# Kernel optimization log

Measured on AMD Instinct MI355X. Metric: run time of the kernel, lower is better.

## Reference

```python
import jax, jax.numpy as jnp
import numpy as np

B, S, D, H = 8, 2048, 1024, 8
CHUNK = D // H
SCALE = float(D) ** (-0.5)  # key_dim ** -0.5, key_dim == num_units here
LN_EPS = 1e-5


def setup_inputs() -> dict:
    key = jax.random.key(0)
    ks = jax.random.split(key, 9)
    s = 0.02
    return {
        "query": jax.random.normal(ks[0], (B, S, D), jnp.float32),
        "keys": jax.random.normal(ks[1], (B, S, D), jnp.float32),
        "Wq": jax.random.normal(ks[2], (D, D), jnp.float32) * s,  # torch Linear weight [out,in]
        "Wk": jax.random.normal(ks[3], (D, D), jnp.float32) * s,
        "Wv": jax.random.normal(ks[4], (D, D), jnp.float32) * s,
        "Wp": jax.random.normal(ks[5], (D, D), jnp.float32) * s,
        "bp": jnp.zeros((D,), jnp.float32),
        "ln_gamma": jnp.ones((D,), jnp.float32),
        "ln_beta": jnp.zeros((D,), jnp.float32),
    }


def reference(query, keys, Wq, Wk, Wv, Wp, bp, ln_gamma, ln_beta):
    # Linear layers (no bias on q/k/v): y = x @ W.T
    Q = jnp.einsum("bsd,ed->bse", query, Wq)
    K = jnp.einsum("bsd,ed->bse", keys, Wk)
    V = jnp.einsum("bsd,ed->bse", keys, Wv)
    # Faithful to original: raw view to [B*h, S, chunk] (no transpose head split)
    Qh = Q.reshape(B * H, S, CHUNK)
    Kh = K.reshape(B * H, S, CHUNK)
    Vh = V.reshape(B * H, S, CHUNK)
    # scores [B*h, S, S], scale, softmax (is_masked=False, dropout_p=0)
    att = jnp.einsum("gqc,gkc->gqk", Qh, Kh) * SCALE
    att = jax.nn.softmax(att, axis=-1)
    ctx = jnp.einsum("gqk,gkc->gqc", att, Vh).reshape(B, S, D)
    # output projection + residual + LayerNorm
    out = jnp.einsum("bsd,ed->bse", ctx, Wp) + bp
    out = out + query
    mu = jnp.mean(out, axis=-1, keepdims=True)
    var = jnp.mean(jnp.square(out - mu), axis=-1, keepdims=True)
    out = (out - mu) * jax.lax.rsqrt(var + LN_EPS) * ln_gamma + ln_beta
    return out
```

## Files before the change

kernel.cpp:

```cpp
#include <hip/hip_runtime.h>

typedef __bf16 bf16x8 __attribute__((ext_vector_type(8)));
typedef float f32x4 __attribute__((ext_vector_type(4)));

#define SCLOG 0.04508422f

__device__ __forceinline__ unsigned short f2bf(float f) {
  union { float f; unsigned int u; } v;
  v.f = f;
  unsigned int u = v.u;
  u += 0x7fffu + ((u >> 16) & 1u);
  return (unsigned short)(u >> 16);
}

__device__ __forceinline__ unsigned asuint(float f) {
  union { float f; unsigned u; } v; v.f = f; return v.u;
}

__device__ __forceinline__ void gld_lds16(const void* g, void* l) {
  __builtin_amdgcn_global_load_lds(
      (const __attribute__((address_space(1))) void*)g,
      (__attribute__((address_space(3))) void*)l, 16, 0, 0);
}

__global__ __launch_bounds__(256) void convert_kernel(
    const float* __restrict__ q, const float* __restrict__ k,
    const float* __restrict__ wq, const float* __restrict__ wk,
    const float* __restrict__ wv, const float* __restrict__ wp,
    unsigned short* __restrict__ qb, unsigned short* __restrict__ kb,
    unsigned short* __restrict__ Wqkv, unsigned short* __restrict__ Wpb) {
  size_t i = (size_t)blockIdx.x * 256 + threadIdx.x;
  const float* src; unsigned short* dst; size_t off;
  if (i < 4194304)      { src = q;  dst = qb;             off = i; }
  else if (i < 8388608) { src = k;  dst = kb;             off = i - 4194304; }
  else if (i < 8650752) { src = wq; dst = Wqkv;           off = i - 8388608; }
  else if (i < 8912896) { src = wk; dst = Wqkv + 1048576; off = i - 8650752; }
  else if (i < 9175040) { src = wv; dst = Wqkv + 2097152; off = i - 8912896; }
  else                  { src = wp; dst = Wpb;            off = i - 9175040; }
  float4 v = ((const float4*)src)[off];
  ushort4 o;
  o.x = f2bf(v.x); o.y = f2bf(v.y); o.z = f2bf(v.z); o.w = f2bf(v.w);
  ((ushort4*)dst)[off] = o;
}

#define QKV_BAR __builtin_amdgcn_s_barrier()
#define QKV_LGKM asm volatile("s_waitcnt lgkmcnt(0)" ::: "memory")

#define QKV_STG(lc, h, srcb, s)                                               \
  gld_lds16((srcb) + (size_t)(s) * 128 + gro0, (lc) + (h) * 16384 + d0);      \
  gld_lds16((srcb) + (size_t)(s) * 128 + gro1, (lc) + (h) * 16384 + d0 + 1024);

#define QKV_RDA(I0)                                                           \
  _Pragma("unroll") for (int i4 = 0; i4 < 4; ++i4) {                          \
    af[i4][0] = *(const bf16x8*)(tb + rbA + ((I0) + i4) * 2048 + cx0);        \
    af[i4][1] = *(const bf16x8*)(tb + rbA + ((I0) + i4) * 2048 + cx1);        \
  }

#define QKV_RDB(JP)                                                           \
  _Pragma("unroll") for (int j2 = 0; j2 < 2; ++j2) {                          \
    bfr[JP][j2][0] = *(const bf16x8*)(tb + rbB + ((JP) * 2 + j2) * 2048 + cx0); \
    bfr[JP][j2][1] = *(const bf16x8*)(tb + rbB + ((JP) * 2 + j2) * 2048 + cx1); \
  }

#define QKV_MM(I0, JP)                                                        \
  _Pragma("unroll") for (int i4 = 0; i4 < 4; ++i4)                            \
  _Pragma("unroll") for (int j2 = 0; j2 < 2; ++j2)                            \
  _Pragma("unroll") for (int kk = 0; kk < 2; ++kk)                            \
    acc[(I0) + i4][(JP) * 2 + j2] = __builtin_amdgcn_mfma_f32_16x16x32_bf16(  \
        af[i4][kk], bfr[JP][j2][kk], acc[(I0) + i4][(JP) * 2 + j2], 0, 0, 0);

__global__ __launch_bounds__(512, 2) void gemm_qkv8_kernel(
    const unsigned short* __restrict__ qb,
    const unsigned short* __restrict__ kb,
    const unsigned short* __restrict__ W,
    unsigned short* __restrict__ Qo,
    unsigned short* __restrict__ Ko,
    unsigned short* __restrict__ Vo) {
  __shared__ char lds[131072];

  const int t = threadIdx.x;
  const int lane = t & 63;
  const int w = t >> 6;
  const int fr = lane & 15;
  const int quad = lane >> 4;

  const int orig = blockIdx.x;
  const int sseq = orig >> 3;
  const int tn = sseq >> 3;
  const int tm = (orig & 7) * 8 + (sseq & 7);

  const unsigned short* Ap = (tn < 4) ? qb : kb;
  const char* aBase = (const char*)Ap + (size_t)(tm * 256) * 2048;
  const char* bBase = (const char*)W + (size_t)(tn * 256) * 2048;

  const int wm2 = w >> 2, wn4 = w & 3;

  const size_t gro0 = (size_t)(w * 16 + (lane >> 3)) * 2048 + (size_t)(((lane & 7) ^ (lane >> 3)) << 4);
  const size_t gro1 = gro0 + 8 * 2048;
  const int d0 = w * 2048 + lane * 16;

  const int rbA = (wm2 * 128 + fr) * 128;
  const int rbB = 32768 + (wn4 * 64 + fr) * 128;
  const int cx0 = (quad * 16) ^ ((fr & 7) << 4);
  const int cx1 = cx0 ^ 64;

  f32x4 acc[8][4];
#pragma unroll
  for (int i = 0; i < 8; ++i)
#pragma unroll
    for (int j = 0; j < 4; ++j) acc[i][j] = (f32x4){0.f, 0.f, 0.f, 0.f};

#pragma unroll
  for (int s = 0; s < 2; ++s) {
    char* lc = lds + s * 65536;
    QKV_STG(lc, 0, aBase, s);
    QKV_STG(lc, 1, aBase + 262144, s);
    QKV_STG(lc + 32768, 0, bBase, s);
    QKV_STG(lc + 32768, 1, bBase + 262144, s);
  }
  asm volatile("s_waitcnt vmcnt(8)" ::: "memory");
  QKV_BAR;

#pragma unroll 1
  for (int kt = 0; kt < 16; ++kt) {
    const char* tb = lds + (kt & 1) * 65536;
    char* lc = lds + (kt & 1) * 65536;
    const int s = kt + 2;
    bf16x8 af[4][2], bfr[2][2][2];

    QKV_RDA(0);
    QKV_RDB(0);
    QKV_BAR; QKV_LGKM;
    __builtin_amdgcn_s_setprio(1);
    QKV_MM(0, 0);
    __builtin_amdgcn_s_setprio(0);
    QKV_BAR;

    QKV_RDB(1);
    QKV_BAR; QKV_LGKM;
    __builtin_amdgcn_s_setprio(1);
    QKV_MM(0, 1);
    __builtin_amdgcn_s_setprio(0);
    QKV_BAR;

    QKV_RDA(4);
    if (s < 16) {
      QKV_STG(lc + 32768, 0, bBase, s);
      QKV_STG(lc + 32768, 1, bBase + 262144, s);
    }
    QKV_BAR; QKV_LGKM;
    __builtin_amdgcn_s_setprio(1);
    QKV_MM(4, 1);
    __builtin_amdgcn_s_setprio(0);
    QKV_BAR;

    if (s < 16) {
      QKV_STG(lc, 0, aBase, s);
      QKV_STG(lc, 1, aBase + 262144, s);
    }
    QKV_BAR;
    __builtin_amdgcn_s_setprio(1);
    QKV_MM(4, 0);
    __builtin_amdgcn_s_setprio(0);
    if (kt <= 13)      { asm volatile("s_waitcnt vmcnt(8)" ::: "memory"); }
    else if (kt == 14) { asm volatile("s_waitcnt vmcnt(0)" ::: "memory"); }
    if (kt < 15) QKV_BAR;
  }

  const int sel = tn >> 2;
  unsigned short* Out = sel == 0 ? Qo : (sel == 1 ? Ko : Vo);
  const int row0 = tm * 256 + wm2 * 128 + quad * 4;
  const int col0 = (tn & 3) * 256 + wn4 * 64 + fr;
#pragma unroll
  for (int i = 0; i < 8; ++i)
#pragma unroll
    for (int j = 0; j < 4; ++j)
#pragma unroll
      for (int r = 0; r < 4; ++r)
        Out[(size_t)(row0 + i * 16 + r) * 1024 + col0 + j * 16] = f2bf(acc[i][j][r]);
}

__global__ __launch_bounds__(256) void vtrans_kernel(
    const unsigned short* __restrict__ V, unsigned short* __restrict__ Vt) {
  __shared__ unsigned short T[128 * 136];
  const int g  = blockIdx.x >> 4;
  const int kt = blockIdx.x & 15;
  const unsigned short* Vg = V + (size_t)g * 262144 + (size_t)kt * 128 * 128;
  unsigned short* Vtg = Vt + (size_t)g * 262144 + kt * 128;
  const int t = threadIdx.x;
#pragma unroll
  for (int it = 0; it < 8; it++) {
    int seg = t + it * 256;
    int k  = seg >> 4;
    int c8 = (seg & 15) << 3;
    uint4 a = *(const uint4*)(Vg + k * 128 + c8);
    unsigned short* Tp = &T[c8 * 136 + k];
    Tp[0 * 136] = (unsigned short)(a.x & 0xffff);
    Tp[1 * 136] = (unsigned short)(a.x >> 16);
    Tp[2 * 136] = (unsigned short)(a.y & 0xffff);
    Tp[3 * 136] = (unsigned short)(a.y >> 16);
    Tp[4 * 136] = (unsigned short)(a.z & 0xffff);
    Tp[5 * 136] = (unsigned short)(a.z >> 16);
    Tp[6 * 136] = (unsigned short)(a.w & 0xffff);
    Tp[7 * 136] = (unsigned short)(a.w >> 16);
  }
  __syncthreads();
#pragma unroll
  for (int it = 0; it < 8; it++) {
    int seg = t + it * 256;
    int c  = seg >> 4;
    int k8 = (seg & 15) << 3;
    uint4 o = *(const uint4*)&T[c * 136 + k8];
    *(uint4*)(Vtg + (size_t)c * 2048 + k8) = o;
  }
}

__global__ __launch_bounds__(512, 4) void attn_kernel(
    const unsigned short* __restrict__ Q,
    const unsigned short* __restrict__ K,
    const unsigned short* __restrict__ Vt,
    unsigned short* __restrict__ ctx) {
  __shared__ unsigned char smem[81920];
  unsigned char* Psh = smem + 65536;

  const int g  = blockIdx.x >> 4;
  const int qt = blockIdx.x & 15;
  const unsigned short* Qg = Q + (size_t)g * 262144 + (size_t)qt * 16384;
  const unsigned short* Kg = K + (size_t)g * 262144;
  const unsigned short* Vg = Vt + (size_t)g * 262144;

  const int t    = threadIdx.x;
  const int lane = t & 63;
  const int wv   = t >> 6;
  const int fr   = lane & 15;
  const int quad = lane >> 4;

#pragma unroll
  for (int it = 0; it < 4; it++) {
    int seg = t + it * 512;
    int r = seg >> 4, p = seg & 15;
    int c = (p & 8) | ((p ^ r) & 7);
    gld_lds16(Qg + r * 128 + c * 8, smem + seg * 16);
  }
  __syncthreads();
  bf16x8 qf[4];
#pragma unroll
  for (int kc = 0; kc < 4; kc++) {
    int row = wv * 16 + fr;
    int c = kc * 4 + quad;
    int p = (c & 8) | ((c ^ (row & 7)) & 7);
    qf[kc] = *(const bf16x8*)(smem + row * 256 + p * 16);
  }
  __syncthreads();

#pragma unroll
  for (int it = 0; it < 2; it++) {
    int seg = t + it * 512;
    int r = seg >> 4, p = seg & 15;
    int c = (p & 8) | ((p ^ r) & 7);
    gld_lds16(Kg + (size_t)r * 128 + c * 8, smem + seg * 16);
  }
#pragma unroll
  for (int it = 0; it < 2; it++) {
    int seg = t + it * 512;
    int r = seg >> 3, p = seg & 7;
    int c = p ^ (r & 7);
    gld_lds16(Vg + (size_t)r * 2048 + c * 8, smem + 32768 + seg * 16);
  }
  __syncthreads();

  f32x4 O[8];
#pragma unroll
  for (int cb = 0; cb < 8; cb++) O[cb] = (f32x4){0.f, 0.f, 0.f, 0.f};
  float lp = 0.f;

#pragma unroll 1
  for (int kt = 0; kt < 32; kt++) {
    unsigned char* Ksh = smem + (unsigned)(kt & 1) * 16384;
    unsigned char* Vsh = smem + 32768 + (unsigned)(kt & 1) * 16384;

    if (kt < 31) {
      unsigned char* Kst = smem + (unsigned)((kt + 1) & 1) * 16384;
      unsigned char* Vst = smem + 32768 + (unsigned)((kt + 1) & 1) * 16384;
#pragma unroll
      for (int it = 0; it < 2; it++) {
        int seg = t + it * 512;
        int r = seg >> 4, p = seg & 15;
        int c = (p & 8) | ((p ^ r) & 7);
        gld_lds16(Kg + (size_t)((kt + 1) * 64 + r) * 128 + c * 8, Kst + seg * 16);
      }
#pragma unroll
      for (int it = 0; it < 2; it++) {
        int seg = t + it * 512;
        int r = seg >> 3, p = seg & 7;
        int c = p ^ (r & 7);
        gld_lds16(Vg + (size_t)r * 2048 + (kt + 1) * 64 + c * 8, Vst + seg * 16);
      }
    }

#pragma unroll
    for (int mt = 0; mt < 4; mt++) {
      bf16x8 kf[4];
#pragma unroll
      for (int kc = 0; kc < 4; kc++) {
        int row = mt * 16 + fr;
        int c = kc * 4 + quad;
        int p = (c & 8) | ((c ^ (row & 7)) & 7);
        kf[kc] = *(const bf16x8*)(Ksh + row * 256 + p * 16);
      }
      f32x4 s = (f32x4){0.f, 0.f, 0.f, 0.f};
#pragma unroll
      for (int kc = 0; kc < 4; kc++)
        s = __builtin_amdgcn_mfma_f32_16x16x32_bf16(kf[kc], qf[kc], s, 0, 0, 0);
      float p0 = exp2f(fminf(s[0] * SCLOG, 30.f));
      float p1 = exp2f(fminf(s[1] * SCLOG, 30.f));
      float p2 = exp2f(fminf(s[2] * SCLOG, 30.f));
      float p3 = exp2f(fminf(s[3] * SCLOG, 30.f));
      lp += (p0 + p1) + (p2 + p3);
      unsigned u01 = __builtin_amdgcn_perm(asuint(p1) + 0x8000u, asuint(p0) + 0x8000u, 0x07060302u);
      unsigned u23 = __builtin_amdgcn_perm(asuint(p3) + 0x8000u, asuint(p2) + 0x8000u, 0x07060302u);
      int qrow = wv * 16 + fr;
      int cP = mt * 2 + (quad >> 1);
      int pP = cP ^ (qrow & 7);
      uint2 u2; u2.x = u01; u2.y = u23;
      *(uint2*)(Psh + qrow * 128 + pP * 16 + (quad & 1) * 8) = u2;
    }

    bf16x8 pf[2];
#pragma unroll
    for (int k2 = 0; k2 < 2; k2++) {
      int qrow = wv * 16 + fr;
      int c = k2 * 4 + quad;
      int p = c ^ (qrow & 7);
      pf[k2] = *(const bf16x8*)(Psh + qrow * 128 + p * 16);
    }
#pragma unroll
    for (int cb = 0; cb < 8; cb++)
#pragma unroll
      for (int k2 = 0; k2 < 2; k2++) {
        int crow = cb * 16 + fr;
        int c = k2 * 4 + quad;
        int p = c ^ (crow & 7);
        bf16x8 vf = *(const bf16x8*)(Vsh + crow * 128 + p * 16);
        O[cb] = __builtin_amdgcn_mfma_f32_16x16x32_bf16(pf[k2], vf, O[cb], 0, 0, 0);
      }

    __syncthreads();
  }

  float* linv_arr = (float*)(smem + 65536);
  {
    float v = lp;
    v += __shfl_xor(v, 16);
    v += __shfl_xor(v, 32);
    if (quad == 0) linv_arr[wv * 16 + fr] = 1.f / v;
  }
  unsigned short* Cg = ctx + (size_t)g * 262144 + (size_t)qt * 16384;
  float li[4];
#pragma unroll
  for (int r = 0; r < 4; r++) li[r] = linv_arr[wv * 16 + quad * 4 + r];
#pragma unroll
  for (int cb = 0; cb < 8; cb++)
#pragma unroll
    for (int r = 0; r < 4; r++) {
      int qrow = wv * 16 + quad * 4 + r;
      Cg[(size_t)qrow * 128 + cb * 16 + fr] = f2bf(O[cb][r] * li[r]);
    }
}

__global__ __launch_bounds__(256) void gemm_proj_kernel(
    const unsigned short* __restrict__ A,
    const unsigned short* __restrict__ W,
    const float* __restrict__ bp,
    const float* __restrict__ qres,
    float* __restrict__ out) {
  __shared__ unsigned short Alds[128 * 32];
  __shared__ unsigned short Blds[128 * 32];
  const int t   = threadIdx.x;
  const int bid = blockIdx.x;
  const int tn  = bid % 8;
  const int tm  = bid / 8;
  const unsigned short* Bptr = W + (size_t)tn * 128 * 1024;

  const int lane = t & 63;
  const int wv   = t >> 6;
  const int wm   = (wv >> 1) * 64;
  const int wn   = (wv & 1) * 64;
  const int fr   = lane & 15;
  const int kq   = (lane >> 4) * 8;

  f32x4 acc[4][4];
#pragma unroll
  for (int i = 0; i < 4; i++)
#pragma unroll
    for (int j = 0; j < 4; j++) acc[i][j] = (f32x4){0.f, 0.f, 0.f, 0.f};

  const int sr = t >> 2;
  const int sc = (t & 3) << 3;
  const unsigned short* gA = A + (size_t)(tm * 128 + sr) * 1024 + sc;
  const unsigned short* gB = Bptr + (size_t)sr * 1024 + sc;
  unsigned short* lA = Alds + t * 8;
  unsigned short* lB = Blds + t * 8;

  for (int k0 = 0; k0 < 1024; k0 += 32) {
    gld_lds16(gA, lA);
    gld_lds16(gA + 64 * 1024, lA + 64 * 32);
    gld_lds16(gB, lB);
    gld_lds16(gB + 64 * 1024, lB + 64 * 32);
    gA += 32; gB += 32;
    __syncthreads();
    bf16x8 af[4], bfr[4];
#pragma unroll
    for (int i = 0; i < 4; i++) {
      af[i]  = *(const bf16x8*)&Alds[(wm + i * 16 + fr) * 32 + kq];
      bfr[i] = *(const bf16x8*)&Blds[(wn + i * 16 + fr) * 32 + kq];
    }
#pragma unroll
    for (int i = 0; i < 4; i++)
#pragma unroll
      for (int j = 0; j < 4; j++)
        acc[i][j] = __builtin_amdgcn_mfma_f32_16x16x32_bf16(af[i], bfr[j], acc[i][j], 0, 0, 0);
    __syncthreads();
  }

  const int quad = lane >> 4;
  const int cc   = lane & 15;
#pragma unroll
  for (int i = 0; i < 4; i++)
#pragma unroll
    for (int j = 0; j < 4; j++)
#pragma unroll
      for (int r = 0; r < 4; r++) {
        int row = tm * 128 + wm + i * 16 + quad * 4 + r;
        int col = tn * 128 + wn + j * 16 + cc;
        out[(size_t)row * 1024 + col] =
            acc[i][j][r] + bp[col] + qres[(size_t)row * 1024 + col];
      }
}

__global__ __launch_bounds__(256) void ln_kernel(float* __restrict__ out,
                                                 const float* __restrict__ gamma,
                                                 const float* __restrict__ beta) {
  __shared__ float red[8];
  const int row = blockIdx.x;
  float* p = out + (size_t)row * 1024;
  const int t = threadIdx.x;
  float4 v = ((const float4*)p)[t];
  float s  = v.x + v.y + v.z + v.w;
  float s2 = v.x * v.x + v.y * v.y + v.z * v.z + v.w * v.w;
#pragma unroll
  for (int off = 1; off < 64; off <<= 1) {
    s  += __shfl_xor(s, off);
    s2 += __shfl_xor(s2, off);
  }
  const int wv = t >> 6;
  if ((t & 63) == 0) { red[wv] = s; red[4 + wv] = s2; }
  __syncthreads();
  float S  = red[0] + red[1] + red[2] + red[3];
  float S2 = red[4] + red[5] + red[6] + red[7];
  float mu  = S * (1.f / 1024.f);
  float var = S2 * (1.f / 1024.f) - mu * mu;
  float rstd = rsqrtf(var + 1e-5f);
  float4 gm = ((const float4*)gamma)[t];
  float4 bt = ((const float4*)beta)[t];
  v.x = (v.x - mu) * rstd * gm.x + bt.x;
  v.y = (v.y - mu) * rstd * gm.y + bt.y;
  v.z = (v.z - mu) * rstd * gm.z + bt.z;
  v.w = (v.w - mu) * rstd * gm.w + bt.w;
  ((float4*)p)[t] = v;
}

extern "C" void kernel_launch(void* const* d_in, const int* in_sizes, int n_in,
                              void* d_out, int out_size, void* d_ws, size_t ws_size,
                              hipStream_t stream) {
  const float* query = (const float*)d_in[0];
  const float* keys  = (const float*)d_in[1];
  const float* Wq    = (const float*)d_in[2];
  const float* Wk    = (const float*)d_in[3];
  const float* Wv    = (const float*)d_in[4];
  const float* Wp    = (const float*)d_in[5];
  const float* bp    = (const float*)d_in[6];
  const float* gamma = (const float*)d_in[7];
  const float* beta  = (const float*)d_in[8];
  float* out = (float*)d_out;

  unsigned short* ws   = (unsigned short*)d_ws;
  unsigned short* qb   = ws;
  unsigned short* kb   = ws + 16777216;
  unsigned short* Wqkv = ws + 33554432;
  unsigned short* Wpb  = ws + 36700160;
  unsigned short* Qb   = ws + 37748736;
  unsigned short* Kb   = ws + 54525952;
  unsigned short* Vb   = ws + 71303168;
  unsigned short* Vtb  = kb;
  unsigned short* ctx  = qb;

  convert_kernel<<<36864, 256, 0, stream>>>(query, keys, Wq, Wk, Wv, Wp, qb, kb, Wqkv, Wpb);
  gemm_qkv8_kernel<<<768, 512, 0, stream>>>(qb, kb, Wqkv, Qb, Kb, Vb);
  vtrans_kernel<<<1024, 256, 0, stream>>>(Vb, Vtb);
  attn_kernel<<<1024, 512, 0, stream>>>(Qb, Kb, Vtb, ctx);
  gemm_proj_kernel<<<1024, 256, 0, stream>>>(ctx, Wpb, bp, query, out);
  ln_kernel<<<16384, 256, 0, stream>>>(out, gamma, beta);
}
```

Baseline: 564.5 us.

## Fold softmax scale into Q projection and streamline attention inner loop

The softmax log2 scale is folded into the Q projection epilogue, which removes a multiply per score in the attention kernel. The attention loop is unrolled by two with fixed double buffers, and LDS and global offsets are precomputed outside the loop to cut per-iteration address arithmetic. Exponentials now use the hardware exp2 intrinsic and bf16 packing uses v_cvt_pk_bf16_f32. Q is rounded to bf16 after scaling, which slightly changes rounding, and the precomputed offsets raise register pressure.

```diff
diff --git a/kernel.cpp b/kernel.cpp
--- a/kernel.cpp
+++ b/kernel.cpp
@@ -11,10 +11,6 @@
   unsigned int u = v.u;
   u += 0x7fffu + ((u >> 16) & 1u);
   return (unsigned short)(u >> 16);
-}
-
-__device__ __forceinline__ unsigned asuint(float f) {
-  union { float f; unsigned u; } v; v.f = f; return v.u;
 }
 
 __device__ __forceinline__ void gld_lds16(const void* g, void* l) {
@@ -169,6 +165,7 @@
 
   const int sel = tn >> 2;
   unsigned short* Out = sel == 0 ? Qo : (sel == 1 ? Ko : Vo);
+  const float osc = (sel == 0) ? SCLOG : 1.f;
   const int row0 = tm * 256 + wm2 * 128 + quad * 4;
   const int col0 = (tn & 3) * 256 + wn4 * 64 + fr;
 #pragma unroll
@@ -177,7 +174,7 @@
     for (int j = 0; j < 4; ++j)
 #pragma unroll
       for (int r = 0; r < 4; ++r)
-        Out[(size_t)(row0 + i * 16 + r) * 1024 + col0 + j * 16] = f2bf(acc[i][j][r]);
+        Out[(size_t)(row0 + i * 16 + r) * 1024 + col0 + j * 16] = f2bf(acc[i][j][r] * osc);
 }
 
 __global__ __launch_bounds__(256) void vtrans_kernel(
@@ -215,6 +212,50 @@
   }
 }
 
+#define ATTN_TILE(KSH, VSH, KST, VST, PREF)                                    \
+  {                                                                            \
+    if (PREF) {                                                                \
+      gld_lds16(kp + kS0, (KST) + kD0);                                        \
+      gld_lds16(kp + kS1, (KST) + kD1);                                        \
+      gld_lds16(vp + vS0, (VST) + vD0);                                        \
+      gld_lds16(vp + vS1, (VST) + vD1);                                        \
+      kp += 8192; vp += 64;                                                    \
+    }                                                                          \
+    _Pragma("unroll")                                                          \
+    for (int mt = 0; mt < 4; mt++) {                                           \
+      bf16x8 kf[4];                                                            \
+      _Pragma("unroll")                                                        \
+      for (int kc = 0; kc < 4; kc++)                                           \
+        kf[kc] = *(const bf16x8*)((KSH) + kfO[mt][kc]);                        \
+      f32x4 s = (f32x4){0.f, 0.f, 0.f, 0.f};                                   \
+      _Pragma("unroll")                                                        \
+      for (int kc = 0; kc < 4; kc++)                                           \
+        s = __builtin_amdgcn_mfma_f32_16x16x32_bf16(kf[kc], qf[kc], s, 0, 0, 0);\
+      float e0 = __builtin_amdgcn_exp2f(fminf(s[0], 30.f));                    \
+      float e1 = __builtin_amdgcn_exp2f(fminf(s[1], 30.f));                    \
+      float e2 = __builtin_amdgcn_exp2f(fminf(s[2], 30.f));                    \
+      float e3 = __builtin_amdgcn_exp2f(fminf(s[3], 30.f));                    \
+      lp += (e0 + e1) + (e2 + e3);                                             \
+      unsigned u01, u23;                                                       \
+      asm("v_cvt_pk_bf16_f32 %0, %1, %2" : "=v"(u01) : "v"(e0), "v"(e1));      \
+      asm("v_cvt_pk_bf16_f32 %0, %1, %2" : "=v"(u23) : "v"(e2), "v"(e3));      \
+      uint2 u2; u2.x = u01; u2.y = u23;                                        \
+      *(uint2*)(Psh + pWr[mt]) = u2;                                           \
+    }                                                                          \
+    {                                                                          \
+      bf16x8 pf0 = *(const bf16x8*)(Psh + pRd0);                               \
+      bf16x8 pf1 = *(const bf16x8*)(Psh + pRd1);                               \
+      _Pragma("unroll")                                                        \
+      for (int cb = 0; cb < 8; cb++) {                                         \
+        O[cb] = __builtin_amdgcn_mfma_f32_16x16x32_bf16(                       \
+            pf0, *(const bf16x8*)((VSH) + vfO[cb][0]), O[cb], 0, 0, 0);        \
+        O[cb] = __builtin_amdgcn_mfma_f32_16x16x32_bf16(                       \
+            pf1, *(const bf16x8*)((VSH) + vfO[cb][1]), O[cb], 0, 0, 0);        \
+      }                                                                        \
+    }                                                                          \
+    __syncthreads();                                                           \
+  }
+
 __global__ __launch_bounds__(512, 4) void attn_kernel(
     const unsigned short* __restrict__ Q,
     const unsigned short* __restrict__ K,
@@ -234,6 +275,54 @@
   const int wv   = t >> 6;
   const int fr   = lane & 15;
   const int quad = lane >> 4;
+  const int qrow = wv * 16 + fr;
+
+  int kfO[4][4];
+#pragma unroll
+  for (int mt = 0; mt < 4; mt++)
+#pragma unroll
+    for (int kc = 0; kc < 4; kc++) {
+      int row = mt * 16 + fr;
+      int c = kc * 4 + quad;
+      int p = (c & 8) | ((c ^ (row & 7)) & 7);
+      kfO[mt][kc] = row * 256 + p * 16;
+    }
+  int vfO[8][2];
+#pragma unroll
+  for (int cb = 0; cb < 8; cb++)
+#pragma unroll
+    for (int k2 = 0; k2 < 2; k2++) {
+      int crow = cb * 16 + fr;
+      int c = k2 * 4 + quad;
+      int p = c ^ (crow & 7);
+      vfO[cb][k2] = crow * 128 + p * 16;
+    }
+  int pWr[4];
+#pragma unroll
+  for (int mt = 0; mt < 4; mt++) {
+    int cP = mt * 2 + (quad >> 1);
+    int pP = cP ^ (qrow & 7);
+    pWr[mt] = qrow * 128 + pP * 16 + (quad & 1) * 8;
+  }
+  int pRd0, pRd1;
+  {
+    int c0 = quad,     p0 = c0 ^ (qrow & 7);
+    int c1 = 4 + quad, p1 = c1 ^ (qrow & 7);
+    pRd0 = qrow * 128 + p0 * 16;
+    pRd1 = qrow * 128 + p1 * 16;
+  }
+  int kS0, kS1, kD0, kD1, vS0, vS1, vD0, vD1;
+  {
+    int seg0 = t, seg1 = t + 512;
+    int r0 = seg0 >> 4, p0 = seg0 & 15, c0 = (p0 & 8) | ((p0 ^ r0) & 7);
+    int r1 = seg1 >> 4, p1 = seg1 & 15, c1 = (p1 & 8) | ((p1 ^ r1) & 7);
+    kS0 = r0 * 128 + c0 * 8;  kD0 = seg0 * 16;
+    kS1 = r1 * 128 + c1 * 8;  kD1 = seg1 * 16;
+    int vr0 = seg0 >> 3, vp0 = seg0 & 7, vc0 = vp0 ^ (vr0 & 7);
+    int vr1 = seg1 >> 3, vp1 = seg1 & 7, vc1 = vp1 ^ (vr1 & 7);
+    vS0 = vr0 * 2048 + vc0 * 8;  vD0 = seg0 * 16;
+    vS1 = vr1 * 2048 + vc1 * 8;  vD1 = seg1 * 16;
+  }
 
 #pragma unroll
   for (int it = 0; it < 4; it++) {
@@ -246,106 +335,35 @@
   bf16x8 qf[4];
 #pragma unroll
   for (int kc = 0; kc < 4; kc++) {
-    int row = wv * 16 + fr;
     int c = kc * 4 + quad;
-    int p = (c & 8) | ((c ^ (row & 7)) & 7);
-    qf[kc] = *(const bf16x8*)(smem + row * 256 + p * 16);
+    int p = (c & 8) | ((c ^ (qrow & 7)) & 7);
+    qf[kc] = *(const bf16x8*)(smem + qrow * 256 + p * 16);
   }
   __syncthreads();
 
-#pragma unroll
-  for (int it = 0; it < 2; it++) {
-    int seg = t + it * 512;
-    int r = seg >> 4, p = seg & 15;
-    int c = (p & 8) | ((p ^ r) & 7);
-    gld_lds16(Kg + (size_t)r * 128 + c * 8, smem + seg * 16);
-  }
-#pragma unroll
-  for (int it = 0; it < 2; it++) {
-    int seg = t + it * 512;
-    int r = seg >> 3, p = seg & 7;
-    int c = p ^ (r & 7);
-    gld_lds16(Vg + (size_t)r * 2048 + c * 8, smem + 32768 + seg * 16);
-  }
+  gld_lds16(Kg + kS0, smem + kD0);
+  gld_lds16(Kg + kS1, smem + kD1);
+  gld_lds16(Vg + vS0, smem + 32768 + vD0);
+  gld_lds16(Vg + vS1, smem + 32768 + vD1);
   __syncthreads();
+
+  const unsigned short* kp = Kg + 8192;
+  const unsigned short* vp = Vg + 64;
 
   f32x4 O[8];
 #pragma unroll
   for (int cb = 0; cb < 8; cb++) O[cb] = (f32x4){0.f, 0.f, 0.f, 0.f};
   float lp = 0.f;
 
+  unsigned char* B0K = smem;
+  unsigned char* B1K = smem + 16384;
+  unsigned char* B0V = smem + 32768;
+  unsigned char* B1V = smem + 49152;
+
 #pragma unroll 1
-  for (int kt = 0; kt < 32; kt++) {
-    unsigned char* Ksh = smem + (unsigned)(kt & 1) * 16384;
-    unsigned char* Vsh = smem + 32768 + (unsigned)(kt & 1) * 16384;
-
-    if (kt < 31) {
-      unsigned char* Kst = smem + (unsigned)((kt + 1) & 1) * 16384;
-      unsigned char* Vst = smem + 32768 + (unsigned)((kt + 1) & 1) * 16384;
-#pragma unroll
-      for (int it = 0; it < 2; it++) {
-        int seg = t + it * 512;
-        int r = seg >> 4, p = seg & 15;
-        int c = (p & 8) | ((p ^ r) & 7);
-        gld_lds16(Kg + (size_t)((kt + 1) * 64 + r) * 128 + c * 8, Kst + seg * 16);
-      }
-#pragma unroll
-      for (int it = 0; it < 2; it++) {
-        int seg = t + it * 512;
-        int r = seg >> 3, p = seg & 7;
-        int c = p ^ (r & 7);
-        gld_lds16(Vg + (size_t)r * 2048 + (kt + 1) * 64 + c * 8, Vst + seg * 16);
-      }
-    }
-
-#pragma unroll
-    for (int mt = 0; mt < 4; mt++) {
-      bf16x8 kf[4];
-#pragma unroll
-      for (int kc = 0; kc < 4; kc++) {
-        int row = mt * 16 + fr;
-        int c = kc * 4 + quad;
-        int p = (c & 8) | ((c ^ (row & 7)) & 7);
-        kf[kc] = *(const bf16x8*)(Ksh + row * 256 + p * 16);
-      }
-      f32x4 s = (f32x4){0.f, 0.f, 0.f, 0.f};
-#pragma unroll
-      for (int kc = 0; kc < 4; kc++)
-        s = __builtin_amdgcn_mfma_f32_16x16x32_bf16(kf[kc], qf[kc], s, 0, 0, 0);
-      float p0 = exp2f(fminf(s[0] * SCLOG, 30.f));
-      float p1 = exp2f(fminf(s[1] * SCLOG, 30.f));
-      float p2 = exp2f(fminf(s[2] * SCLOG, 30.f));
-      float p3 = exp2f(fminf(s[3] * SCLOG, 30.f));
-      lp += (p0 + p1) + (p2 + p3);
-      unsigned u01 = __builtin_amdgcn_perm(asuint(p1) + 0x8000u, asuint(p0) + 0x8000u, 0x07060302u);
-      unsigned u23 = __builtin_amdgcn_perm(asuint(p3) + 0x8000u, asuint(p2) + 0x8000u, 0x07060302u);
-      int qrow = wv * 16 + fr;
-      int cP = mt * 2 + (quad >> 1);
-      int pP = cP ^ (qrow & 7);
-      uint2 u2; u2.x = u01; u2.y = u23;
-      *(uint2*)(Psh + qrow * 128 + pP * 16 + (quad & 1) * 8) = u2;
-    }
-
-    bf16x8 pf[2];
-#pragma unroll
-    for (int k2 = 0; k2 < 2; k2++) {
-      int qrow = wv * 16 + fr;
-      int c = k2 * 4 + quad;
-      int p = c ^ (qrow & 7);
-      pf[k2] = *(const bf16x8*)(Psh + qrow * 128 + p * 16);
-    }
-#pragma unroll
-    for (int cb = 0; cb < 8; cb++)
-#pragma unroll
-      for (int k2 = 0; k2 < 2; k2++) {
-        int crow = cb * 16 + fr;
-        int c = k2 * 4 + quad;
-        int p = c ^ (crow & 7);
-        bf16x8 vf = *(const bf16x8*)(Vsh + crow * 128 + p * 16);
-        O[cb] = __builtin_amdgcn_mfma_f32_16x16x32_bf16(pf[k2], vf, O[cb], 0, 0, 0);
-      }
-
-    __syncthreads();
+  for (int kt2 = 0; kt2 < 16; kt2++) {
+    ATTN_TILE(B0K, B0V, B1K, B1V, 1);
+    ATTN_TILE(B1K, B1V, B0K, B0V, (kt2 < 15));
   }
 
   float* linv_arr = (float*)(smem + 65536);
@@ -363,8 +381,8 @@
   for (int cb = 0; cb < 8; cb++)
 #pragma unroll
     for (int r = 0; r < 4; r++) {
-      int qrow = wv * 16 + quad * 4 + r;
-      Cg[(size_t)qrow * 128 + cb * 16 + fr] = f2bf(O[cb][r] * li[r]);
+      int orow = wv * 16 + quad * 4 + r;
+      Cg[(size_t)orow * 128 + cb * 16 + fr] = f2bf(O[cb][r] * li[r]);
     }
 }
 
```

Result: faster. 542.7 us (-3.9%).
